# Kernel optimization log

Measured on AMD Instinct MI355X. Metric: run time of the kernel, lower is better.

Reference implementation:

```python
import jax, jax.numpy as jnp
import numpy as np


def setup_inputs() -> dict:
    key = jax.random.key(0)
    k1, k2, k3 = jax.random.split(key, 3)
    N, C, H, W, S = 9, 32, 192, 256, 9  # 1 ref + 8 src views, 3x3 patch samples
    f = jax.random.normal(k1, (N, C, H, W, S), dtype=jnp.float32)
    Wp = jax.random.normal(k2, (C, C), dtype=jnp.float32) / np.sqrt(C)  # Conv1d(C,C,1) weight
    bp = jax.random.normal(k3, (C,), dtype=jnp.float32) * 0.01  # Conv1d bias
    return {"f": f, "Wp": Wp, "bp": bp, "o": 2, "G": 8}


def reference(f, Wp, bp, o, G):
    # f: (N, C, H, W, S); view 0 is the reference image, views 1..N-1 are sources.
    N, C, H, W, S = f.shape
    ref = f[0]          # (C, H, W, S)
    src = f[1:]         # (N-1, C, H, W, S)

    # 1x1 Conv1d projection of the reference patches (per-position linear).
    proj = jnp.einsum('dc,chws->dhws', Wp, ref) + bp[:, None, None, None]  # (C,H,W,S)

    # Dot-product attention of the center sample (S//2) against all S samples.
    logits = jnp.sum(proj[:, :, :, S // 2, None] * proj, axis=0) / jnp.sqrt(jnp.float32(C))  # (H,W,S)
    att = jax.nn.softmax(logits, axis=-1)  # (H,W,S)

    # Grouped correlation: split channels into G groups of Cg, dot within each group.
    Cg = C // G
    ref_g = ref.reshape(G, Cg, H, W, S)
    src_g = src.reshape(N - 1, G, Cg, H, W, S)
    gc = jnp.einsum('gchws,ngchws->nghws', ref_g, src_g)  # (N-1, G, H, W, S)

    # Attention-weighted reduction over the S patch-sample axis.
    return jnp.sum(gc * att[None, None], axis=-1)  # (N-1, G, H, W)
```

## Files before the change

### kernel.cpp

```cpp
#include <hip/hip_runtime.h>
#include <math.h>

#define NSRC 8
#define CCH  32
#define HH   192
#define WW   256
#define SS   9
#define GG   8

#define F_SC (HH*WW*SS)
#define F_SH (WW*SS)
#define F_SN (CCH*HH*WW*SS)

#define WS_M   0
#define WS_V   1024
#define WS_BB  1056
#define WS_ATT 1064

__global__ void k0_precompute(const float* __restrict__ Wp,
                              const float* __restrict__ bp,
                              float* __restrict__ ws) {
    const float inv_sqrtC = 0.17677669529663687f;
    int t = threadIdx.x;
    for (int idx = t; idx < 1024; idx += 256) {
        int c = idx >> 5, c2 = idx & 31;
        float acc = 0.f;
        for (int d = 0; d < 32; ++d) acc = fmaf(Wp[d*32 + c], Wp[d*32 + c2], acc);
        ws[WS_M + idx] = acc * inv_sqrtC;
    }
    if (t < 32) {
        float acc = 0.f;
        for (int d = 0; d < 32; ++d) acc = fmaf(Wp[d*32 + t], bp[d], acc);
        ws[WS_V + t] = acc * inv_sqrtC;
    }
    if (t == 0) {
        float acc = 0.f;
        for (int d = 0; d < 32; ++d) acc = fmaf(bp[d], bp[d], acc);
        ws[WS_BB] = acc * inv_sqrtC;
    }
}

__global__ __launch_bounds__(64) void k1_att(const float* __restrict__ f,
                                             const float* __restrict__ ws,
                                             float* __restrict__ att_out) {
    int p = blockIdx.x * 64 + threadIdx.x;
    int h = p >> 8;
    int w = p & 255;
    const long base = (long)h * F_SH + (long)w * SS;

    float u[32];
    #pragma unroll
    for (int c = 0; c < 32; ++c) u[c] = ws[WS_V + c];
    float beta = ws[WS_BB];

    for (int cp = 0; cp < 32; ++cp) {
        float r4 = f[(long)cp * F_SC + base + 4];
        beta = fmaf(r4, ws[WS_V + cp], beta);
        #pragma unroll
        for (int c = 0; c < 32; ++c)
            u[c] = fmaf(ws[WS_M + c * 32 + cp], r4, u[c]);
    }

    float lg[SS];
    #pragma unroll
    for (int s = 0; s < SS; ++s) lg[s] = beta;
    for (int c = 0; c < 32; ++c) {
        const float* rrow = f + (long)c * F_SC + base;
        float uc = u[c];
        #pragma unroll
        for (int s = 0; s < SS; ++s) lg[s] = fmaf(uc, rrow[s], lg[s]);
    }

    float m = lg[0];
    #pragma unroll
    for (int s = 1; s < SS; ++s) m = fmaxf(m, lg[s]);
    float e[SS], sum = 0.f;
    #pragma unroll
    for (int s = 0; s < SS; ++s) { e[s] = __expf(lg[s] - m); sum += e[s]; }
    float inv = 1.f / sum;
    #pragma unroll
    for (int s = 0; s < SS; ++s) att_out[(long)p * SS + s] = e[s] * inv;
}

__global__ __launch_bounds__(256) void k2_out(const float* __restrict__ f,
                                              const float* __restrict__ att,
                                              float* __restrict__ out) {
    int t  = threadIdx.x;
    int wi = t & 31;
    int n  = t >> 5;
    int w  = blockIdx.x * 32 + wi;
    int h  = blockIdx.y;
    const long pix  = (long)h * WW + w;
    const long base = (long)h * F_SH + (long)w * SS;

    float a[SS];
    #pragma unroll
    for (int s = 0; s < SS; ++s) a[s] = att[pix * SS + s];

    const float* refp = f + base;
    const float* srcp = f + (long)(n + 1) * F_SN + base;

    float acc[GG];
    #pragma unroll
    for (int g = 0; g < GG; ++g) {
        float ag = 0.f;
        #pragma unroll
        for (int cc = 0; cc < 4; ++cc) {
            int c = g * 4 + cc;
            const float* rr = refp + (long)c * F_SC;
            const float* sr = srcp + (long)c * F_SC;
            #pragma unroll
            for (int s = 0; s < SS; ++s) {
                float ar = a[s] * rr[s];
                ag = fmaf(ar, sr[s], ag);
            }
        }
        acc[g] = ag;
    }

    #pragma unroll
    for (int g = 0; g < GG; ++g)
        out[(((long)n * GG + g) * HH + h) * WW + w] = acc[g];
}

extern "C" void kernel_launch(void* const* d_in, const int* in_sizes, int n_in,
                              void* d_out, int out_size, void* d_ws, size_t ws_size,
                              hipStream_t stream) {
    const float* f  = (const float*)d_in[0];
    const float* Wp = (const float*)d_in[1];
    const float* bp = (const float*)d_in[2];
    float* out = (float*)d_out;
    float* ws  = (float*)d_ws;
    float* att = ws + WS_ATT;

    k0_precompute<<<1, 256, 0, stream>>>(Wp, bp, ws);

    k1_att<<<768, 64, 0, stream>>>(f, ws, att);

    k2_out<<<dim3(WW / 32, HH), 256, 0, stream>>>(f, att, out);
}
```

Baseline: 689.7 us.

## Fuse attention and grouped-correlation kernels with shared-memory ref patches

Merges the attention kernel and the output kernel into one block-per-row-segment kernel. The reference patches are loaded once into shared memory and reused by all 8 source-view warps. The attention logit computation is split across warps by channel and reduced through shared memory. This removes the separate pass over the reference view, the attention round-trip to global memory and one launch, at the cost of more shared memory per block and extra barriers.

```diff
diff --git a/kernel.cpp b/kernel.cpp
--- a/kernel.cpp
+++ b/kernel.cpp
@@ -15,7 +15,6 @@
 #define WS_M   0
 #define WS_V   1024
 #define WS_BB  1056
-#define WS_ATT 1064
 
 __global__ void k0_precompute(const float* __restrict__ Wp,
                               const float* __restrict__ bp,
@@ -40,81 +39,122 @@
     }
 }
 
-__global__ __launch_bounds__(64) void k1_att(const float* __restrict__ f,
-                                             const float* __restrict__ ws,
-                                             float* __restrict__ att_out) {
-    int p = blockIdx.x * 64 + threadIdx.x;
-    int h = p >> 8;
-    int w = p & 255;
+__global__ __launch_bounds__(256) void k_fused(const float* __restrict__ f,
+                                               const float* __restrict__ ws,
+                                               float* __restrict__ out) {
+    __shared__ float ref_s[CCH * SS][32];
+    __shared__ float M_s[1024];
+    __shared__ float v_s[32];
+    __shared__ float bb_s;
+    __shared__ float lgp[32][8][SS];
+    __shared__ float pbeta[32][8];
+    __shared__ float att_s[32][SS];
+
+    const int t  = threadIdx.x;
+    const int wi = t & 31;
+    const int n  = t >> 5;
+    const int w  = blockIdx.x * 32 + wi;
+    const int h  = blockIdx.y;
     const long base = (long)h * F_SH + (long)w * SS;
 
-    float u[32];
+    ((float4*)M_s)[t] = ((const float4*)(ws + WS_M))[t];
+    if (t < 32) v_s[t] = ws[WS_V + t];
+    if (t == 0) bb_s = ws[WS_BB];
+
+    float rref[4 * SS];
+    const float* refp = f + base;
     #pragma unroll
-    for (int c = 0; c < 32; ++c) u[c] = ws[WS_V + c];
-    float beta = ws[WS_BB];
+    for (int cc = 0; cc < 4; ++cc) {
+        const int c = 4 * n + cc;
+        const float* rr = refp + (long)c * F_SC;
+        #pragma unroll
+        for (int s = 0; s < SS; ++s) {
+            float v = rr[s];
+            rref[cc * SS + s] = v;
+            ref_s[c * SS + s][wi] = v;
+        }
+    }
+    __syncthreads();
 
+    float pb = 0.f;
+    #pragma unroll
+    for (int cc = 0; cc < 4; ++cc)
+        pb = fmaf(rref[cc * SS + 4], v_s[4 * n + cc], pb);
+    pbeta[wi][n] = pb;
+
+    float u[4];
+    #pragma unroll
+    for (int cc = 0; cc < 4; ++cc) u[cc] = v_s[4 * n + cc];
     for (int cp = 0; cp < 32; ++cp) {
-        float r4 = f[(long)cp * F_SC + base + 4];
-        beta = fmaf(r4, ws[WS_V + cp], beta);
+        float r4 = ref_s[cp * SS + 4][wi];
         #pragma unroll
-        for (int c = 0; c < 32; ++c)
-            u[c] = fmaf(ws[WS_M + c * 32 + cp], r4, u[c]);
+        for (int cc = 0; cc < 4; ++cc)
+            u[cc] = fmaf(M_s[(4 * n + cc) * 32 + cp], r4, u[cc]);
     }
 
-    float lg[SS];
+    float lgv[SS];
     #pragma unroll
-    for (int s = 0; s < SS; ++s) lg[s] = beta;
-    for (int c = 0; c < 32; ++c) {
-        const float* rrow = f + (long)c * F_SC + base;
-        float uc = u[c];
+    for (int s = 0; s < SS; ++s) lgv[s] = 0.f;
+    #pragma unroll
+    for (int cc = 0; cc < 4; ++cc) {
+        float uc = u[cc];
         #pragma unroll
-        for (int s = 0; s < SS; ++s) lg[s] = fmaf(uc, rrow[s], lg[s]);
+        for (int s = 0; s < SS; ++s)
+            lgv[s] = fmaf(uc, rref[cc * SS + s], lgv[s]);
     }
+    #pragma unroll
+    for (int s = 0; s < SS; ++s) lgp[wi][n][s] = lgv[s];
+    __syncthreads();
 
-    float m = lg[0];
-    #pragma unroll
-    for (int s = 1; s < SS; ++s) m = fmaxf(m, lg[s]);
-    float e[SS], sum = 0.f;
-    #pragma unroll
-    for (int s = 0; s < SS; ++s) { e[s] = __expf(lg[s] - m); sum += e[s]; }
-    float inv = 1.f / sum;
-    #pragma unroll
-    for (int s = 0; s < SS; ++s) att_out[(long)p * SS + s] = e[s] * inv;
-}
+    if (n == 0) {
+        float lt[SS];
+        float beta = bb_s;
+        #pragma unroll
+        for (int nn = 0; nn < 8; ++nn) beta += pbeta[wi][nn];
+        #pragma unroll
+        for (int s = 0; s < SS; ++s) lt[s] = beta;
+        #pragma unroll
+        for (int nn = 0; nn < 8; ++nn)
+            #pragma unroll
+            for (int s = 0; s < SS; ++s) lt[s] += lgp[wi][nn][s];
 
-__global__ __launch_bounds__(256) void k2_out(const float* __restrict__ f,
-                                              const float* __restrict__ att,
-                                              float* __restrict__ out) {
-    int t  = threadIdx.x;
-    int wi = t & 31;
-    int n  = t >> 5;
-    int w  = blockIdx.x * 32 + wi;
-    int h  = blockIdx.y;
-    const long pix  = (long)h * WW + w;
-    const long base = (long)h * F_SH + (long)w * SS;
+        float m = lt[0];
+        #pragma unroll
+        for (int s = 1; s < SS; ++s) m = fmaxf(m, lt[s]);
+        float e[SS], sum = 0.f;
+        #pragma unroll
+        for (int s = 0; s < SS; ++s) { e[s] = __expf(lt[s] - m); sum += e[s]; }
+        float inv = 1.f / sum;
+        #pragma unroll
+        for (int s = 0; s < SS; ++s) att_s[wi][s] = e[s] * inv;
+    }
+    __syncthreads();
 
     float a[SS];
     #pragma unroll
-    for (int s = 0; s < SS; ++s) a[s] = att[pix * SS + s];
+    for (int s = 0; s < SS; ++s) a[s] = att_s[wi][s];
 
-    const float* refp = f + base;
     const float* srcp = f + (long)(n + 1) * F_SN + base;
 
     float acc[GG];
     #pragma unroll
     for (int g = 0; g < GG; ++g) {
-        float ag = 0.f;
+        float ps[SS];
+        #pragma unroll
+        for (int s = 0; s < SS; ++s) ps[s] = 0.f;
         #pragma unroll
         for (int cc = 0; cc < 4; ++cc) {
-            int c = g * 4 + cc;
-            const float* rr = refp + (long)c * F_SC;
+            const int c = g * 4 + cc;
             const float* sr = srcp + (long)c * F_SC;
             #pragma unroll
             for (int s = 0; s < SS; ++s) {
-                float ar = a[s] * rr[s];
-                ag = fmaf(ar, sr[s], ag);
+                float rv = ref_s[c * SS + s][wi];
+                ps[s] = fmaf(rv, sr[s], ps[s]);
             }
         }
+        float ag = 0.f;
+        #pragma unroll
+        for (int s = 0; s < SS; ++s) ag = fmaf(a[s], ps[s], ag);
         acc[g] = ag;
     }
 
@@ -131,11 +171,7 @@
     const float* bp = (const float*)d_in[2];
     float* out = (float*)d_out;
     float* ws  = (float*)d_ws;
-    float* att = ws + WS_ATT;
 
     k0_precompute<<<1, 256, 0, stream>>>(Wp, bp, ws);
-
-    k1_att<<<768, 64, 0, stream>>>(f, ws, att);
-
-    k2_out<<<dim3(WW / 32, HH), 256, 0, stream>>>(f, att, out);
+    k_fused<<<dim3(WW / 32, HH), 256, 0, stream>>>(f, ws, out);
 }
```

New measurement: 665.0 us. 3.6% less time.
